# Kernel tuning notes

Measured on AMD Instinct MI355X. Metric: run time of the kernel, lower is better.

Reference implementation:

```python
import jax, jax.numpy as jnp
import numpy as np
import math

B, S, CZ, H, CH = 1, 384, 128, 4, 32


def setup_inputs() -> dict:
    key = jax.random.key(0)
    ks = jax.random.split(key, 12)
    sd = 0.02
    return {
        "z": jax.random.normal(ks[0], (B, S, S, CZ), dtype=jnp.float32),
        "ln_w": jnp.ones((CZ,), dtype=jnp.float32),
        "ln_b": jnp.zeros((CZ,), dtype=jnp.float32),
        "Wq": jax.random.normal(ks[1], (H * CH, CZ), dtype=jnp.float32) * sd,
        "Wk": jax.random.normal(ks[2], (CH, CZ), dtype=jnp.float32) * sd,
        "Wv": jax.random.normal(ks[3], (CH, CZ), dtype=jnp.float32) * sd,
        "Wb": jax.random.normal(ks[4], (H, CZ), dtype=jnp.float32) * sd,
        "Wg": jax.random.normal(ks[5], (H * CH, CZ), dtype=jnp.float32) * sd,
        "bg": jnp.zeros((H * CH,), dtype=jnp.float32),
        "Wo": jax.random.normal(ks[6], (CZ, H * CH), dtype=jnp.float32) * sd,
        "bo": jnp.zeros((CZ,), dtype=jnp.float32),
    }


def reference(z, ln_w, ln_b, Wq, Wk, Wv, Wb, Wg, bg, Wo, bo):
    b_, s_, _, cz = z.shape
    h = Wb.shape[0]          # n_heads
    ch = Wk.shape[0]         # c_hidden
    # LayerNorm over c_z (eps = 1e-5, torch default)
    mu = jnp.mean(z, axis=-1, keepdims=True)
    var = jnp.mean(jnp.square(z - mu), axis=-1, keepdims=True)
    zn = (z - mu) * jax.lax.rsqrt(var + 1e-5) * ln_w + ln_b
    # projections (starting=True: attend along rows i over key index k)
    q = (zn @ Wq.T).reshape(b_, s_, s_, h, ch)   # [B,I,J,H,C]
    k = zn @ Wk.T                                 # [B,I,K,C] shared across heads
    v = zn @ Wv.T                                 # [B,I,K,C]
    bias = zn @ Wb.T                              # [B,I,J,H]
    g = jax.nn.sigmoid(zn @ Wg.T + bg)            # [B,I,J,H*C]
    scale = 1.0 / math.sqrt(ch)
    logits = jnp.einsum('bijhc,bikc->bihjk', q, k) * scale  # [B,I,H,J,K]
    # NOTE: faithful to source — bias broadcasts along the KEY axis (softmax-invariant)
    logits = logits + jnp.transpose(bias, (0, 1, 3, 2))[..., None]
    w = jax.nn.softmax(logits, axis=-1)           # [B,I,H,J,K]
    o = jnp.einsum('bihjk,bikc->bijhc', w, v).reshape(b_, s_, s_, h * ch)
    o = g * o
    return o @ Wo.T + bo
```

## Files before the change

### kernel.cpp

```cpp
#include <hip/hip_runtime.h>
#include <math.h>


typedef unsigned short u16;
typedef __attribute__((ext_vector_type(8))) short short8;
typedef __attribute__((ext_vector_type(4))) short short4v;
typedef __attribute__((ext_vector_type(4))) float float4v;

union U8 { short8 s; u16 h[8]; };
union U4 { short4v s; u16 h[4]; };

__device__ __forceinline__ float bf2f(u16 x){
    unsigned v = ((unsigned)x) << 16;
    float f; __builtin_memcpy(&f, &v, 4);
    return f;
}
__device__ __forceinline__ u16 f2bf(float f){
    unsigned v; __builtin_memcpy(&v, &f, 4);
    unsigned r = (v + 0x7FFFu + ((v >> 16) & 1u)) >> 16;
    return (u16)r;
}
__device__ __forceinline__ float exp2_fast(float x){
    float r; asm("v_exp_f32 %0, %1" : "=v"(r) : "v"(x));
    return r;
}
__device__ __forceinline__ short8 pack8f_s(const float* p, float s){
    const float4 a = ((const float4*)p)[0];
    const float4 b = ((const float4*)p)[1];
    U8 u;
    u.h[0]=f2bf(a.x*s); u.h[1]=f2bf(a.y*s); u.h[2]=f2bf(a.z*s); u.h[3]=f2bf(a.w*s);
    u.h[4]=f2bf(b.x*s); u.h[5]=f2bf(b.y*s); u.h[6]=f2bf(b.z*s); u.h[7]=f2bf(b.w*s);
    return u.s;
}

__global__ __launch_bounds__(256) void k0a_wconv(
    const float* __restrict__ Wq, const float* __restrict__ Wk,
    const float* __restrict__ Wv, const float* __restrict__ Wg,
    u16* __restrict__ Wbf)
{
    const int i = blockIdx.x * 256 + threadIdx.x;
    const int e = i * 8;
    const int n = e >> 7, c0 = e & 127;
    const float* src; float s = 1.f;
    if (n < 128)      { src = Wq + n*128 + c0; s = 0.17677669529663689f * 1.4426950408889634f; }
    else if (n < 160) { src = Wk + (n-128)*128 + c0; }
    else if (n < 192) { src = Wv + (n-160)*128 + c0; }
    else              { src = Wg + (n-192)*128 + c0; }
    *(short8*)(Wbf + e) = pack8f_s(src, s);
}

__global__ __launch_bounds__(256) void k0b_wconv(
    const float* __restrict__ Wo, u16* __restrict__ WoBf)
{
    const int e = (blockIdx.x * 256 + threadIdx.x) * 8;
    *(short8*)(WoBf + e) = pack8f_s(Wo + e, 1.f);
}

__global__ __launch_bounds__(256) void k1_ln_proj(
    const float* __restrict__ z, const float* __restrict__ lnw, const float* __restrict__ lnb,
    const u16* __restrict__ Wbf, const float* __restrict__ bg,
    u16* __restrict__ Qbuf, u16* __restrict__ KVbuf, u16* __restrict__ Gbuf)
{
    __shared__ __align__(16) u16 zn[64][136];
    const int tid = threadIdx.x;
    const long rowg0 = (long)blockIdx.x * 64;

    {
        const int r = tid >> 2, p = tid & 3;
        const float* src = z + (rowg0 + r) * 128 + p * 32;
        float x[32];
        #pragma unroll
        for (int q = 0; q < 8; q++){
            const float4 v = ((const float4*)src)[q];
            x[q*4+0]=v.x; x[q*4+1]=v.y; x[q*4+2]=v.z; x[q*4+3]=v.w;
        }
        float s = 0.f, ss = 0.f;
        #pragma unroll
        for (int t = 0; t < 32; t++){ s += x[t]; ss += x[t]*x[t]; }
        s += __shfl_xor(s, 1);  ss += __shfl_xor(ss, 1);
        s += __shfl_xor(s, 2);  ss += __shfl_xor(ss, 2);
        const float mean = s * (1.f/128.f);
        const float var  = ss * (1.f/128.f) - mean*mean;
        const float rstd = rsqrtf(var + 1e-5f);
        #pragma unroll
        for (int t = 0; t < 32; t++){
            const int c = p*32 + t;
            zn[r][c] = f2bf((x[t]-mean)*rstd*lnw[c] + lnb[c]);
        }
    }
    __syncthreads();

    const int lane = tid & 63, wave = tid >> 6;
    const int l15 = lane & 15, quad = lane >> 4;

    short8 ZN[4][4];
    #pragma unroll
    for (int m = 0; m < 4; m++)
        #pragma unroll
        for (int ks = 0; ks < 4; ks++)
            ZN[m][ks] = *(const short8*)&zn[m*16 + l15][ks*32 + quad*8];

    #pragma unroll
    for (int g = 0; g < 5; g++){
        const int nt = wave*5 + g;
        const u16* wp = Wbf + (nt*16 + l15)*128 + quad*8;
        short8 WF[4];
        #pragma unroll
        for (int ks = 0; ks < 4; ks++) WF[ks] = *(const short8*)(wp + ks*32);
        const int n0 = nt*16 + quad*4;
        #pragma unroll
        for (int m = 0; m < 4; m++){
            float4v c = {0.f,0.f,0.f,0.f};
            #pragma unroll
            for (int ks = 0; ks < 4; ks++)
                c = __builtin_amdgcn_mfma_f32_16x16x32_bf16(WF[ks], ZN[m][ks], c, 0, 0, 0);
            const long row = rowg0 + m*16 + l15;
            if (nt < 8){
                U4 u;
                #pragma unroll
                for (int r = 0; r < 4; r++) u.h[r] = f2bf(c[r]);
                *(short4v*)(Qbuf + row*128 + n0) = u.s;
            } else if (nt < 10){
                U4 u;
                #pragma unroll
                for (int r = 0; r < 4; r++) u.h[r] = f2bf(c[r]);
                *(short4v*)(KVbuf + row*64 + (n0 - 128)) = u.s;
            } else if (nt < 12){
                U4 u;
                #pragma unroll
                for (int r = 0; r < 4; r++) u.h[r] = f2bf(c[r]);
                *(short4v*)(KVbuf + row*64 + (n0 - 160) + 32) = u.s;
            } else {
                const float4 b4 = *(const float4*)&bg[n0 - 192];
                U4 u;
                u.h[0] = f2bf(1.f/(1.f + __expf(-(c[0] + b4.x))));
                u.h[1] = f2bf(1.f/(1.f + __expf(-(c[1] + b4.y))));
                u.h[2] = f2bf(1.f/(1.f + __expf(-(c[2] + b4.z))));
                u.h[3] = f2bf(1.f/(1.f + __expf(-(c[3] + b4.w))));
                *(short4v*)(Gbuf + row*128 + (n0 - 192)) = u.s;
            }
        }
    }
}

__global__ __launch_bounds__(512, 4) void k2_attn(
    const u16* __restrict__ KVbuf, const u16* __restrict__ Gbuf, u16* __restrict__ QObuf)
{
    __shared__ __align__(16) u16 Ks[384][40];
    __shared__ __align__(16) u16 Vt[32][392];
    __shared__ __align__(16) u16 Pb[8][16][72];
    const int i = blockIdx.x >> 1, jh = blockIdx.x & 1;
    const int tid = threadIdx.x;
    const u16* kvsrc = KVbuf + (long)i * 384 * 64;
    {
        for (int idx = tid; idx < 384*8; idx += 512){
            const int k = idx >> 3, c8 = idx & 7;
            U8 d; d.s = *(const short8*)(kvsrc + k*64 + c8*8);
            if (c8 < 4) *(short8*)&Ks[k][c8*8] = d.s;
            else {
                const int c0 = (c8 - 4) * 8;
                #pragma unroll
                for (int jj = 0; jj < 8; jj++) Vt[c0 + jj][k] = d.h[jj];
            }
        }
    }
    __syncthreads();

    const int lane = tid & 63, wave = tid >> 6;
    const int l15 = lane & 15, quad = lane >> 4;
    const int h = wave >> 1, sub = wave & 1;
    const u16* qbase = QObuf + (long)i * 384 * 128 + h * 32;
    const u16* gbase = Gbuf  + (long)i * 384 * 128 + h * 32;
    u16* obase = QObuf + (long)i * 384 * 128 + h * 32;

    for (int t = 0; t < 6; t++){
        const int j0 = (jh*12 + sub*6 + t) * 16;
        const short8 aq = *(const short8*)(qbase + (long)(j0 + l15)*128 + quad*8);
        float4v acc[24];
        #pragma unroll
        for (int kt = 0; kt < 24; kt++){
            const short8 bk = *(const short8*)&Ks[kt*16 + l15][quad*8];
            float4v zero = {0.f,0.f,0.f,0.f};
            acc[kt] = __builtin_amdgcn_mfma_f32_16x16x32_bf16(aq, bk, zero, 0, 0, 0);
        }
        float inv[4];
        #pragma unroll
        for (int r = 0; r < 4; r++){
            float mx = -1e30f;
            #pragma unroll
            for (int kt = 0; kt < 24; kt++) mx = fmaxf(mx, acc[kt][r]);
            mx = fmaxf(mx, __shfl_xor(mx, 1));
            mx = fmaxf(mx, __shfl_xor(mx, 2));
            mx = fmaxf(mx, __shfl_xor(mx, 4));
            mx = fmaxf(mx, __shfl_xor(mx, 8));
            float sum = 0.f;
            #pragma unroll
            for (int kt = 0; kt < 24; kt++){ acc[kt][r] = exp2_fast(acc[kt][r] - mx); sum += acc[kt][r]; }
            sum += __shfl_xor(sum, 1);
            sum += __shfl_xor(sum, 2);
            sum += __shfl_xor(sum, 4);
            sum += __shfl_xor(sum, 8);
            inv[r] = 1.f / sum;
        }
        float4v oacc[2] = {{0.f,0.f,0.f,0.f},{0.f,0.f,0.f,0.f}};
        #pragma unroll
        for (int cc = 0; cc < 6; cc++){
            #pragma unroll
            for (int j = 0; j < 4; j++){
                const int kt = cc*4 + j;
                #pragma unroll
                for (int r = 0; r < 4; r++)
                    Pb[wave][quad*4 + r][j*16 + l15] = f2bf(acc[kt][r]);
            }
            #pragma unroll
            for (int kj = 0; kj < 2; kj++){
                const int kk = cc*2 + kj;
                const short8 ap = *(const short8*)&Pb[wave][l15][kj*32 + quad*8];
                #pragma unroll
                for (int ct = 0; ct < 2; ct++){
                    const short8 bv = *(const short8*)&Vt[ct*16 + l15][kk*32 + quad*8];
                    oacc[ct] = __builtin_amdgcn_mfma_f32_16x16x32_bf16(ap, bv, oacc[ct], 0, 0, 0);
                }
            }
        }
        #pragma unroll
        for (int ct = 0; ct < 2; ct++){
            const int c = ct*16 + l15;
            #pragma unroll
            for (int r = 0; r < 4; r++){
                const int row = j0 + quad*4 + r;
                const float gv = bf2f(gbase[(long)row*128 + c]);
                obase[(long)row*128 + c] = f2bf(gv * (oacc[ct][r] * inv[r]));
            }
        }
    }
}

__global__ __launch_bounds__(256) void k3_outproj(
    const u16* __restrict__ Obuf, const u16* __restrict__ WoBf, const float* __restrict__ bo,
    float* __restrict__ out)
{
    const int tid = threadIdx.x, lane = tid & 63, wave = tid >> 6;
    const int l15 = lane & 15, quad = lane >> 4;
    const long row0 = (long)blockIdx.x * 64;
    short8 WF[2][4];
    #pragma unroll
    for (int g = 0; g < 2; g++){
        const u16* wp = WoBf + ((wave*2 + g)*16 + l15)*128 + quad*8;
        #pragma unroll
        for (int ks = 0; ks < 4; ks++) WF[g][ks] = *(const short8*)(wp + ks*32);
    }
    #pragma unroll
    for (int m = 0; m < 4; m++){
        short8 OF[4];
        const u16* ap = Obuf + (row0 + m*16 + l15)*128 + quad*8;
        #pragma unroll
        for (int ks = 0; ks < 4; ks++) OF[ks] = *(const short8*)(ap + ks*32);
        #pragma unroll
        for (int g = 0; g < 2; g++){
            float4v c = {0.f,0.f,0.f,0.f};
            #pragma unroll
            for (int ks = 0; ks < 4; ks++)
                c = __builtin_amdgcn_mfma_f32_16x16x32_bf16(WF[g][ks], OF[ks], c, 0, 0, 0);
            const int n0 = (wave*2 + g)*16 + quad*4;
            const float4 b4 = *(const float4*)&bo[n0];
            const long row = row0 + m*16 + l15;
            float4 o4;
            o4.x = c[0] + b4.x; o4.y = c[1] + b4.y;
            o4.z = c[2] + b4.z; o4.w = c[3] + b4.w;
            *(float4*)(out + row*128 + n0) = o4;
        }
    }
}

extern "C" void kernel_launch(void* const* d_in, const int* in_sizes, int n_in,
                              void* d_out, int out_size, void* d_ws, size_t ws_size,
                              hipStream_t stream)
{
    (void)in_sizes; (void)n_in; (void)out_size; (void)ws_size;
    const float* z   = (const float*)d_in[0];
    const float* lnw = (const float*)d_in[1];
    const float* lnb = (const float*)d_in[2];
    const float* Wq  = (const float*)d_in[3];
    const float* Wk  = (const float*)d_in[4];
    const float* Wv  = (const float*)d_in[5];
    const float* Wg  = (const float*)d_in[7];
    const float* bg  = (const float*)d_in[8];
    const float* Wo  = (const float*)d_in[9];
    const float* bo  = (const float*)d_in[10];

    u16* Qbuf = (u16*)d_ws;
    u16* KV   = Qbuf + 147456L*128;
    u16* Gbuf = (u16*)d_out;
    u16* Wbf  = Gbuf + 147456L*128;
    u16* WoBf = KV;

    k0a_wconv<<<dim3(20), dim3(256), 0, stream>>>(Wq, Wk, Wv, Wg, Wbf);
    k1_ln_proj<<<dim3(2304), dim3(256), 0, stream>>>(z, lnw, lnb, Wbf, bg,
                                                     Qbuf, KV, Gbuf);
    k2_attn<<<dim3(768), dim3(512), 0, stream>>>(KV, Gbuf, Qbuf);
    k0b_wconv<<<dim3(8), dim3(256), 0, stream>>>(Wo, WoBf);
    k3_outproj<<<dim3(2304), dim3(256), 0, stream>>>(Qbuf, WoBf, bo, (float*)d_out);
}
```

Measured before the change: 329.2 us.

## Transpose attention MFMA operands so softmax rows live per lane

Swaps the A/B operands of both MFMAs in the attention kernel so each lane holds four key columns of one query row. Row max and sum then need only two cross-lane shuffles instead of four shuffles per row for each of four rows. P is written to shared memory as packed 8-byte bf16 pairs via v_cvt_pk_bf16_f32 instead of scalar 2-byte stores. The gated output becomes a vectorized 4-element load and store. This relies on the hardware packed-convert instruction, which may round differently from the manual round-to-nearest-even code.

```diff
diff --git a/kernel.cpp b/kernel.cpp
--- a/kernel.cpp
+++ b/kernel.cpp
@@ -6,6 +6,7 @@
 typedef __attribute__((ext_vector_type(8))) short short8;
 typedef __attribute__((ext_vector_type(4))) short short4v;
 typedef __attribute__((ext_vector_type(4))) float float4v;
+typedef __attribute__((ext_vector_type(2))) unsigned uint2v;
 
 union U8 { short8 s; u16 h[8]; };
 union U4 { short4v s; u16 h[4]; };
@@ -22,6 +23,11 @@
 }
 __device__ __forceinline__ float exp2_fast(float x){
     float r; asm("v_exp_f32 %0, %1" : "=v"(r) : "v"(x));
+    return r;
+}
+__device__ __forceinline__ unsigned cvt_pk_bf16(float lo, float hi){
+    unsigned r;
+    asm("v_cvt_pk_bf16_f32 %0, %1, %2" : "=v"(r) : "v"(lo), "v"(hi));
     return r;
 }
 __device__ __forceinline__ short8 pack8f_s(const float* p, float s){
@@ -148,7 +154,7 @@
 {
     __shared__ __align__(16) u16 Ks[384][40];
     __shared__ __align__(16) u16 Vt[32][392];
-    __shared__ __align__(16) u16 Pb[8][16][72];
+    __shared__ __align__(16) u16 Pj[8][16][72];
     const int i = blockIdx.x >> 1, jh = blockIdx.x & 1;
     const int tid = threadIdx.x;
     const u16* kvsrc = KVbuf + (long)i * 384 * 64;
@@ -181,57 +187,65 @@
         for (int kt = 0; kt < 24; kt++){
             const short8 bk = *(const short8*)&Ks[kt*16 + l15][quad*8];
             float4v zero = {0.f,0.f,0.f,0.f};
-            acc[kt] = __builtin_amdgcn_mfma_f32_16x16x32_bf16(aq, bk, zero, 0, 0, 0);
-        }
-        float inv[4];
-        #pragma unroll
-        for (int r = 0; r < 4; r++){
-            float mx = -1e30f;
+            acc[kt] = __builtin_amdgcn_mfma_f32_16x16x32_bf16(bk, aq, zero, 0, 0, 0);
+        }
+        float m0 = -1e30f, m1 = -1e30f, m2 = -1e30f, m3 = -1e30f;
+        #pragma unroll
+        for (int kt = 0; kt < 24; kt++){
+            m0 = fmaxf(m0, acc[kt][0]); m1 = fmaxf(m1, acc[kt][1]);
+            m2 = fmaxf(m2, acc[kt][2]); m3 = fmaxf(m3, acc[kt][3]);
+        }
+        float mx = fmaxf(fmaxf(m0, m1), fmaxf(m2, m3));
+        mx = fmaxf(mx, __shfl_xor(mx, 16));
+        mx = fmaxf(mx, __shfl_xor(mx, 32));
+        float s0 = 0.f, s1 = 0.f, s2 = 0.f, s3 = 0.f;
+        #pragma unroll
+        for (int kt = 0; kt < 24; kt++){
+            acc[kt][0] = exp2_fast(acc[kt][0] - mx); s0 += acc[kt][0];
+            acc[kt][1] = exp2_fast(acc[kt][1] - mx); s1 += acc[kt][1];
+            acc[kt][2] = exp2_fast(acc[kt][2] - mx); s2 += acc[kt][2];
+            acc[kt][3] = exp2_fast(acc[kt][3] - mx); s3 += acc[kt][3];
+        }
+        float sum = (s0 + s1) + (s2 + s3);
+        sum += __shfl_xor(sum, 16);
+        sum += __shfl_xor(sum, 32);
+        const float inv = 1.f / sum;
+
+        float4v oacc[2] = {{0.f,0.f,0.f,0.f},{0.f,0.f,0.f,0.f}};
+        #pragma unroll
+        for (int g6 = 0; g6 < 6; g6++){
             #pragma unroll
-            for (int kt = 0; kt < 24; kt++) mx = fmaxf(mx, acc[kt][r]);
-            mx = fmaxf(mx, __shfl_xor(mx, 1));
-            mx = fmaxf(mx, __shfl_xor(mx, 2));
-            mx = fmaxf(mx, __shfl_xor(mx, 4));
-            mx = fmaxf(mx, __shfl_xor(mx, 8));
-            float sum = 0.f;
-            #pragma unroll
-            for (int kt = 0; kt < 24; kt++){ acc[kt][r] = exp2_fast(acc[kt][r] - mx); sum += acc[kt][r]; }
-            sum += __shfl_xor(sum, 1);
-            sum += __shfl_xor(sum, 2);
-            sum += __shfl_xor(sum, 4);
-            sum += __shfl_xor(sum, 8);
-            inv[r] = 1.f / sum;
-        }
-        float4v oacc[2] = {{0.f,0.f,0.f,0.f},{0.f,0.f,0.f,0.f}};
-        #pragma unroll
-        for (int cc = 0; cc < 6; cc++){
-            #pragma unroll
-            for (int j = 0; j < 4; j++){
-                const int kt = cc*4 + j;
-                #pragma unroll
-                for (int r = 0; r < 4; r++)
-                    Pb[wave][quad*4 + r][j*16 + l15] = f2bf(acc[kt][r]);
+            for (int kk = 0; kk < 4; kk++){
+                const int kt = g6*4 + kk;
+                uint2v d;
+                d.x = cvt_pk_bf16(acc[kt][0], acc[kt][1]);
+                d.y = cvt_pk_bf16(acc[kt][2], acc[kt][3]);
+                *(uint2v*)&Pj[wave][l15][kk*16 + quad*4] = d;
             }
             #pragma unroll
-            for (int kj = 0; kj < 2; kj++){
-                const int kk = cc*2 + kj;
-                const short8 ap = *(const short8*)&Pb[wave][l15][kj*32 + quad*8];
+            for (int kc = 0; kc < 2; kc++){
+                const short8 bp = *(const short8*)&Pj[wave][l15][kc*32 + quad*8];
+                const int ch = g6*2 + kc;
                 #pragma unroll
                 for (int ct = 0; ct < 2; ct++){
-                    const short8 bv = *(const short8*)&Vt[ct*16 + l15][kk*32 + quad*8];
-                    oacc[ct] = __builtin_amdgcn_mfma_f32_16x16x32_bf16(ap, bv, oacc[ct], 0, 0, 0);
+                    const short8 av = *(const short8*)&Vt[ct*16 + l15][ch*32 + quad*8];
+                    oacc[ct] = __builtin_amdgcn_mfma_f32_16x16x32_bf16(av, bp, oacc[ct], 0, 0, 0);
                 }
             }
         }
         #pragma unroll
         for (int ct = 0; ct < 2; ct++){
-            const int c = ct*16 + l15;
-            #pragma unroll
-            for (int r = 0; r < 4; r++){
-                const int row = j0 + quad*4 + r;
-                const float gv = bf2f(gbase[(long)row*128 + c]);
-                obase[(long)row*128 + c] = f2bf(gv * (oacc[ct][r] * inv[r]));
-            }
+            const int c0 = ct*16 + quad*4;
+            const long roff = (long)(j0 + l15)*128 + c0;
+            U4 g4; g4.s = *(const short4v*)(gbase + roff);
+            const float o0 = bf2f(g4.h[0]) * (oacc[ct][0] * inv);
+            const float o1 = bf2f(g4.h[1]) * (oacc[ct][1] * inv);
+            const float o2 = bf2f(g4.h[2]) * (oacc[ct][2] * inv);
+            const float o3 = bf2f(g4.h[3]) * (oacc[ct][3] * inv);
+            uint2v st;
+            st.x = cvt_pk_bf16(o0, o1);
+            st.y = cvt_pk_bf16(o2, o3);
+            *(uint2v*)(obase + roff) = st;
         }
     }
 }
```

After: 452.1 us. +37.3%, slower.
